# Kernel optimization log

Hardware: AMD Instinct MI355X
Metric: run time of the kernel (lower is better)

The kernel has to match this reference:

```python
import jax, jax.numpy as jnp
import numpy as np
import math

D_MODEL = 1024
N_HEADS = 16
D_K = D_MODEL // N_HEADS
WIDTH_MULTIPLIER = 1.0  # readout=False on all projections, so unused in math


def setup_inputs() -> dict:
    key = jax.random.key(0)
    kx, kq, kk, kv, ko = jax.random.split(key, 5)
    std = 1.0 / math.sqrt(D_MODEL)  # init_scale=1.0 / sqrt(in_features)
    x = jax.random.normal(kx, (2, 2048, D_MODEL), dtype=jnp.float32)
    # weights stored as (out_features, in_features), matching torch
    Wq = jax.random.normal(kq, (D_MODEL, D_MODEL), dtype=jnp.float32) * std
    Wk = jax.random.normal(kk, (D_MODEL, D_MODEL), dtype=jnp.float32) * std
    Wv = jax.random.normal(kv, (D_MODEL, D_MODEL), dtype=jnp.float32) * std
    Wo = jax.random.normal(ko, (D_MODEL, D_MODEL), dtype=jnp.float32) * std
    return {"x": x, "Wq": Wq, "Wk": Wk, "Wv": Wv, "Wo": Wo}


def reference(x, Wq, Wk, Wv, Wo):
    B, S, D = x.shape
    H, Dk = N_HEADS, D_K
    # muPLinear: x @ W.T (bias=False, readout=False)
    q = jnp.einsum('bsd,ed->bse', x, Wq).reshape(B, S, H, Dk).transpose(0, 2, 1, 3)
    k = jnp.einsum('bsd,ed->bse', x, Wk).reshape(B, S, H, Dk).transpose(0, 2, 1, 3)
    v = jnp.einsum('bsd,ed->bse', x, Wv).reshape(B, S, H, Dk).transpose(0, 2, 1, 3)
    # full [B,H,S,S] scores, scaled by 1/sqrt(d_k), softmax over keys
    scores = jnp.einsum('bhqd,bhkd->bhqk', q, k) / math.sqrt(Dk)
    attn = jax.nn.softmax(scores, axis=-1)
    out = jnp.einsum('bhqk,bhkd->bhqd', attn, v)
    out = out.transpose(0, 2, 1, 3).reshape(B, S, D)
    return jnp.einsum('bsd,ed->bse', out, Wo)
```

## Files before the change

kernel.cpp:

```cpp
#include <hip/hip_runtime.h>
#include <hip/hip_bf16.h>
#include <math.h>

#define D_MODEL 1024
#define N_HEADS 16
#define D_K     64
#define BATCH   2
#define SEQ     2048
#define M_TOTAL (BATCH * SEQ)

typedef __attribute__((ext_vector_type(8))) short short8;
typedef __attribute__((ext_vector_type(4))) float f32x4;
typedef __attribute__((ext_vector_type(16))) float f32x16;

__device__ __forceinline__ ushort f2bf(float f) {
    __hip_bfloat16 h = __float2bfloat16(f);
    union { __hip_bfloat16 h; ushort u; } c; c.h = h; return c.u;
}

__device__ __forceinline__ uint cvtpk(float a, float b) {
    uint r;
    asm("v_cvt_pk_bf16_f32 %0, %1, %2" : "=v"(r) : "v"(a), "v"(b));
    return r;
}

__device__ __forceinline__ void gload_lds16(const void* g, void* l) {
    __builtin_amdgcn_global_load_lds(
        (const __attribute__((address_space(1))) void*)g,
        (__attribute__((address_space(3))) void*)l, 16, 0, 0);
}

__device__ __forceinline__ void plswap(uint& a, uint& b) {
    asm volatile("v_permlane32_swap_b32 %0, %1" : "+v"(a), "+v"(b));
}

__global__ __launch_bounds__(256) void cast_all(const float* __restrict__ x,
                                                const float* __restrict__ Wq,
                                                const float* __restrict__ Wk,
                                                const float* __restrict__ Wv,
                                                const float* __restrict__ Wo,
                                                ushort* __restrict__ xb,
                                                ushort* __restrict__ wqkv,
                                                ushort* __restrict__ wob)
{
    const int bi = blockIdx.x;
    const float* src; ushort* dst; int blk;
    const int NW = D_MODEL * D_MODEL;
    if (bi < 4096)      { src = x;  dst = xb;            blk = bi; }
    else if (bi < 5120) { src = Wq; dst = wqkv;          blk = bi - 4096; }
    else if (bi < 6144) { src = Wk; dst = wqkv + NW;     blk = bi - 5120; }
    else if (bi < 7168) { src = Wv; dst = wqkv + 2 * NW; blk = bi - 6144; }
    else                { src = Wo; dst = wob;           blk = bi - 7168; }
    const int i = blk * 1024 + threadIdx.x * 4;
    float4 v = *(const float4*)&src[i];
    ushort4 o;
    o.x = f2bf(v.x); o.y = f2bf(v.y); o.z = f2bf(v.z); o.w = f2bf(v.w);
    *(ushort4*)&dst[i] = o;
}

template <int EPI>
__global__ __launch_bounds__(256) void gemm_bf16(const ushort* __restrict__ A,
                                                 const ushort* __restrict__ B,
                                                 void* __restrict__ C0,
                                                 void* __restrict__ C1,
                                                 void* __restrict__ C2,
                                                 int M, int N, int K)
{
    __shared__ ushort As[2][4 * 128 * 8];
    __shared__ ushort Bs[2][4 * 128 * 8];

    const int tid = threadIdx.x;
    const int lane = tid & 63;
    const int w = tid >> 6;
    const int li = lane & 15;
    const int kg = lane >> 4;

    const int nwg = gridDim.x * gridDim.y;
    const int flat = blockIdx.y * gridDim.x + blockIdx.x;
    const int cpx = nwg >> 3;
    const int swz = (flat & 7) * cpx + (flat >> 3);
    const int m0 = (swz / gridDim.x) * 128;
    const int n0 = (swz % gridDim.x) * 128;

    const int wr = (w >> 1) * 64;
    const int wc = (w & 1) * 64;

    f32x4 acc[4][4] = {};

    const int s1 = tid, s2 = tid + 256;
    const ushort* ga1 = &A[(size_t)(m0 + (s1 & 127)) * K + (s1 >> 7) * 8];
    const ushort* ga2 = &A[(size_t)(m0 + (s2 & 127)) * K + (s2 >> 7) * 8];
    const ushort* gb1 = &B[(size_t)(n0 + (s1 & 127)) * K + (s1 >> 7) * 8];
    const ushort* gb2 = &B[(size_t)(n0 + (s2 & 127)) * K + (s2 >> 7) * 8];

    const int NT = K / 32;
    gload_lds16(ga1, &As[0][s1 * 8]);
    gload_lds16(ga2, &As[0][s2 * 8]);
    gload_lds16(gb1, &Bs[0][s1 * 8]);
    gload_lds16(gb2, &Bs[0][s2 * 8]);

    for (int t = 0; t < NT; ++t) {
        const int cur = t & 1;
        asm volatile("s_waitcnt vmcnt(0)" ::: "memory");
        __syncthreads();
        if (t + 1 < NT) {
            const int kb = (t + 1) * 32;
            const int nxt = cur ^ 1;
            gload_lds16(ga1 + kb, &As[nxt][s1 * 8]);
            gload_lds16(ga2 + kb, &As[nxt][s2 * 8]);
            gload_lds16(gb1 + kb, &Bs[nxt][s1 * 8]);
            gload_lds16(gb2 + kb, &Bs[nxt][s2 * 8]);
        }
        short8 af[4], bf_[4];
#pragma unroll
        for (int m = 0; m < 4; ++m)
            af[m] = *(const short8*)&As[cur][(kg * 128 + wr + m * 16 + li) * 8];
#pragma unroll
        for (int n = 0; n < 4; ++n)
            bf_[n] = *(const short8*)&Bs[cur][(kg * 128 + wc + n * 16 + li) * 8];
#pragma unroll
        for (int m = 0; m < 4; ++m)
#pragma unroll
            for (int n = 0; n < 4; ++n)
                acc[m][n] = __builtin_amdgcn_mfma_f32_16x16x32_bf16(
                    af[m], bf_[n], acc[m][n], 0, 0, 0);
    }

    if (EPI == 1) {
        ushort* q = (ushort*)C0; ushort* k = (ushort*)C1; ushort* v = (ushort*)C2;
        const float QSCALE = 0.125f * 1.44269504088896f;
#pragma unroll
        for (int m = 0; m < 4; ++m) {
            const int Rb = m0 + wr + m * 16 + kg * 4;
#pragma unroll
            for (int n = 0; n < 4; ++n) {
                const int Ncol = n0 + wc + n * 16 + li;
                const int proj = Ncol >> 10;
                const int rem = Ncol & 1023;
                const int h = rem >> 6, dk = rem & 63;
#pragma unroll
                for (int r = 0; r < 4; ++r) {
                    const int R = Rb + r;
                    const int b = R >> 11, s = R & 2047;
                    const int bh = b * N_HEADS + h;
                    if (proj == 0)
                        q[((size_t)bh * SEQ + s) * D_K + dk] = f2bf(acc[m][n][r] * QSCALE);
                    else if (proj == 1)
                        k[((size_t)bh * SEQ + s) * D_K + dk] = f2bf(acc[m][n][r]);
                    else
                        v[((size_t)bh * D_K + dk) * SEQ + s] = f2bf(acc[m][n][r]);
                }
            }
        }
    } else {
        float* C = (float*)C0;
#pragma unroll
        for (int m = 0; m < 4; ++m) {
            const int Rb = m0 + wr + m * 16 + kg * 4;
#pragma unroll
            for (int n = 0; n < 4; ++n) {
                const int Ncol = n0 + wc + n * 16 + li;
#pragma unroll
                for (int r = 0; r < 4; ++r)
                    C[(size_t)(Rb + r) * N + Ncol] = acc[m][n][r];
            }
        }
    }
}

__global__ __launch_bounds__(512, 4) void attn_mfma(const ushort* __restrict__ Q,
                                                    const ushort* __restrict__ K,
                                                    const ushort* __restrict__ Vt,
                                                    ushort* __restrict__ AO)
{
    __shared__ ushort pool[2][2][2][64 * 64];

    const int tid = threadIdx.x, lane = tid & 63, w = tid >> 6;
    const int wq = w & 3, kvh = w >> 2;
    const int r31 = lane & 31, hi = lane >> 5;
    const int b = blockIdx.z, h = blockIdx.y, q0 = blockIdx.x * 128;
    const int bh = b * N_HEADS + h;
    const size_t base = (size_t)bh * SEQ * D_K;
    const size_t vbase = (size_t)bh * D_K * SEQ;

    uint pa = (uint)lane, pbv = 1000u + (uint)lane;
    plswap(pa, pbv);
    const bool swap_lo = (__builtin_amdgcn_readfirstlane(pa) > 500u);

    const size_t qrow = base + (size_t)(q0 + wq * 32 + r31) * D_K;
    short8 qb[4];
#pragma unroll
    for (int ks = 0; ks < 4; ++ks)
        qb[ks] = *(const short8*)&Q[qrow + ks * 16 + hi * 8];

    float m_ = -INFINITY, l_ = 0.f;
    f32x16 o0 = {}, o1 = {};

    const int srow_l = lane >> 3;
    const int sblk = lane & 7;
    const ushort* Kt0 = &K[base];
    const ushort* Vt0 = &Vt[vbase];
    const int tile0 = kvh * 16;

    const int xr = r31 & 7;
    int off[2][4];
#pragma unroll
    for (int hf = 0; hf < 2; ++hf)
#pragma unroll
        for (int ks = 0; ks < 4; ++ks)
            off[hf][ks] = hf * 2048 + r31 * 64 + (((2 * ks + hi) ^ xr) * 8);

    const ushort* Kst = &pool[kvh][0][0][0];
    const ushort* Vst = &pool[kvh][1][0][0];

#define STAGE(kt_, buf_)                                                       \
    {                                                                          \
        _Pragma("unroll")                                                      \
        for (int p = 0; p < 2; ++p) {                                          \
            const int row = wq * 16 + p * 8 + srow_l;                          \
            const int db = sblk ^ (row & 7);                                   \
            gload_lds16(Kt0 + ((size_t)((tile0 + (kt_)) * 64 + row)) * D_K + db * 8, \
                        &pool[kvh][0][buf_][(wq * 16 + p * 8) * 64]);          \
            gload_lds16(Vt0 + (size_t)row * SEQ + (tile0 + (kt_)) * 64 + db * 8,     \
                        &pool[kvh][1][buf_][(wq * 16 + p * 8) * 64]);          \
        }                                                                      \
    }

    STAGE(0, 0);

    const int NT = SEQ / 64 / 2;
    for (int kt = 0; kt < NT; ++kt) {
        const int cur = kt & 1;
        asm volatile("s_waitcnt vmcnt(0)" ::: "memory");
        __syncthreads();
        if (kt + 1 < NT) STAGE(kt + 1, cur ^ 1);
        const int cb = cur * 4096;

        f32x16 s0 = {}, s1 = {};
        __builtin_amdgcn_s_setprio(1);
#pragma unroll
        for (int ks = 0; ks < 4; ++ks) {
            short8 kb = *(const short8*)(Kst + cb + off[0][ks]);
            s0 = __builtin_amdgcn_mfma_f32_32x32x16_bf16(kb, qb[ks], s0, 0, 0, 0);
        }
#pragma unroll
        for (int ks = 0; ks < 4; ++ks) {
            short8 kb = *(const short8*)(Kst + cb + off[1][ks]);
            s1 = __builtin_amdgcn_mfma_f32_32x32x16_bf16(kb, qb[ks], s1, 0, 0, 0);
        }
        __builtin_amdgcn_s_setprio(0);

        float mx = fmaxf(s0[0], s0[1]);
#pragma unroll
        for (int e = 2; e < 16; ++e) mx = fmaxf(mx, s0[e]);
#pragma unroll
        for (int e = 0; e < 16; ++e) mx = fmaxf(mx, s1[e]);
        mx = fmaxf(mx, __shfl_xor(mx, 32, 64));

        if (__any(mx > m_ + 8.0f)) {
            const float mn = fmaxf(m_, mx);
            const float sc = exp2f(m_ - mn);
            l_ *= sc;
#pragma unroll
            for (int e = 0; e < 16; ++e) { o0[e] *= sc; o1[e] *= sc; }
            m_ = mn;
        }

        f32x16 p0, p1;
        float ts = 0.f;
#pragma unroll
        for (int e = 0; e < 16; ++e) { p0[e] = exp2f(s0[e] - m_); ts += p0[e]; }
#pragma unroll
        for (int e = 0; e < 16; ++e) { p1[e] = exp2f(s1[e] - m_); ts += p1[e]; }
        ts += __shfl_xor(ts, 32, 64);
        l_ += ts;

        uint u[8][2];
#pragma unroll
        for (int rq = 0; rq < 4; ++rq) {
            u[rq][0]     = cvtpk(p0[4 * rq + 0], p0[4 * rq + 1]);
            u[rq][1]     = cvtpk(p0[4 * rq + 2], p0[4 * rq + 3]);
            u[4 + rq][0] = cvtpk(p1[4 * rq + 0], p1[4 * rq + 1]);
            u[4 + rq][1] = cvtpk(p1[4 * rq + 2], p1[4 * rq + 3]);
        }

        short8 pb[4];
#pragma unroll
        for (int ks = 0; ks < 4; ++ks) {
            uint x0 = u[2 * ks][0], x1 = u[2 * ks][1];
            uint y0 = u[2 * ks + 1][0], y1 = u[2 * ks + 1][1];
            if (swap_lo) { plswap(y0, x0); plswap(y1, x1); }
            else         { plswap(x0, y0); plswap(x1, y1); }
            union { uint u4[4]; short8 s; } pu;
            pu.u4[0] = x0; pu.u4[1] = x1; pu.u4[2] = y0; pu.u4[3] = y1;
            pb[ks] = pu.s;
        }

        __builtin_amdgcn_s_setprio(1);
#pragma unroll
        for (int ks = 0; ks < 4; ++ks) {
            short8 vb = *(const short8*)(Vst + cb + off[0][ks]);
            o0 = __builtin_amdgcn_mfma_f32_32x32x16_bf16(vb, pb[ks], o0, 0, 0, 0);
        }
#pragma unroll
        for (int ks = 0; ks < 4; ++ks) {
            short8 vb = *(const short8*)(Vst + cb + off[1][ks]);
            o1 = __builtin_amdgcn_mfma_f32_32x32x16_bf16(vb, pb[ks], o1, 0, 0, 0);
        }
        __builtin_amdgcn_s_setprio(0);
    }
#undef STAGE

    __syncthreads();
    float* cs = (float*)&pool[0][0][0][0];
    float* ml = cs + 4 * 64 * 32;
    const int cidx = (wq * 64 + lane) * 32;
    if (kvh == 1) {
#pragma unroll
        for (int rq = 0; rq < 4; ++rq) {
            f32x4 a, c;
#pragma unroll
            for (int e = 0; e < 4; ++e) { a[e] = o0[4 * rq + e]; c[e] = o1[4 * rq + e]; }
            *(f32x4*)&cs[cidx + 4 * rq] = a;
            *(f32x4*)&cs[cidx + 16 + 4 * rq] = c;
        }
        ml[(wq * 64 + lane) * 2]     = m_;
        ml[(wq * 64 + lane) * 2 + 1] = l_;
    }
    __syncthreads();
    if (kvh == 0) {
        const float m2 = ml[(wq * 64 + lane) * 2];
        const float l2 = ml[(wq * 64 + lane) * 2 + 1];
        const float mM = fmaxf(m_, m2);
        const float sc1 = exp2f(m_ - mM), sc2 = exp2f(m2 - mM);
        const float linv = 1.f / (l_ * sc1 + l2 * sc2);
        ushort* Ao = &AO[((size_t)b * SEQ + q0 + wq * 32 + r31) * D_MODEL + h * 64];
#pragma unroll
        for (int rq = 0; rq < 4; ++rq) {
            f32x4 a = *(const f32x4*)&cs[cidx + 4 * rq];
            f32x4 c = *(const f32x4*)&cs[cidx + 16 + 4 * rq];
            uint2 v0, v1;
            v0.x = cvtpk((o0[4 * rq + 0] * sc1 + a[0] * sc2) * linv,
                         (o0[4 * rq + 1] * sc1 + a[1] * sc2) * linv);
            v0.y = cvtpk((o0[4 * rq + 2] * sc1 + a[2] * sc2) * linv,
                         (o0[4 * rq + 3] * sc1 + a[3] * sc2) * linv);
            v1.x = cvtpk((o1[4 * rq + 0] * sc1 + c[0] * sc2) * linv,
                         (o1[4 * rq + 1] * sc1 + c[1] * sc2) * linv);
            v1.y = cvtpk((o1[4 * rq + 2] * sc1 + c[2] * sc2) * linv,
                         (o1[4 * rq + 3] * sc1 + c[3] * sc2) * linv);
            *(uint2*)&Ao[8 * rq + 4 * hi]      = v0;
            *(uint2*)&Ao[32 + 8 * rq + 4 * hi] = v1;
        }
    }
}

extern "C" void kernel_launch(void* const* d_in, const int* in_sizes, int n_in,
                              void* d_out, int out_size, void* d_ws, size_t ws_size,
                              hipStream_t stream)
{
    const float* x  = (const float*)d_in[0];
    const float* Wq = (const float*)d_in[1];
    const float* Wk = (const float*)d_in[2];
    const float* Wv = (const float*)d_in[3];
    const float* Wo = (const float*)d_in[4];
    float* out = (float*)d_out;

    ushort* xb   = (ushort*)d_ws;
    ushort* Wqkv = xb + (size_t)M_TOTAL * D_MODEL;
    ushort* Wob  = Wqkv + (size_t)3 * D_MODEL * D_MODEL;
    ushort* q    = Wob + (size_t)D_MODEL * D_MODEL;
    ushort* k    = q + (size_t)M_TOTAL * D_MODEL;
    ushort* vt   = k + (size_t)M_TOTAL * D_MODEL;
    ushort* ao   = vt + (size_t)M_TOTAL * D_MODEL;

    hipLaunchKernelGGL(cast_all, dim3(8192), dim3(256), 0, stream,
                       x, Wq, Wk, Wv, Wo, xb, Wqkv, Wob);

    hipLaunchKernelGGL((gemm_bf16<1>), dim3(3 * D_MODEL / 128, M_TOTAL / 128), dim3(256),
                       0, stream, xb, Wqkv, q, k, vt, M_TOTAL, 3 * D_MODEL, D_MODEL);

    hipLaunchKernelGGL(attn_mfma, dim3(SEQ / 128, N_HEADS, BATCH), dim3(512),
                       0, stream, q, k, vt, ao);

    hipLaunchKernelGGL((gemm_bf16<0>), dim3(D_MODEL / 128, M_TOTAL / 128), dim3(256),
                       0, stream, ao, Wob, out, (void*)0, (void*)0,
                       M_TOTAL, D_MODEL, D_MODEL);
}
```

Before: 166.8 us.

## Stage V-transpose epilogue through LDS and shrink output GEMM tile to 64 rows

In the QKV projection GEMM, the V-projection tiles now write their accumulators into a swizzled LDS buffer and then emit the transposed V layout with coalesced 16-byte stores. Previously each element was a scattered 2-byte store strided by SEQ. The output projection GEMM becomes a separate kernel with 64x128 tiles. That doubles its workgroup count from 256 to 512 to improve CU occupancy on the small N=1024 problem. The cost is an extra LDS round trip and two barriers in the V epilogue, plus lower per-block reuse in the output GEMM.

```diff
diff --git a/kernel.cpp b/kernel.cpp
--- a/kernel.cpp
+++ b/kernel.cpp
@@ -58,22 +58,20 @@
     *(ushort4*)&dst[i] = o;
 }
 
-template <int EPI>
-__global__ __launch_bounds__(256) void gemm_bf16(const ushort* __restrict__ A,
-                                                 const ushort* __restrict__ B,
-                                                 void* __restrict__ C0,
-                                                 void* __restrict__ C1,
-                                                 void* __restrict__ C2,
-                                                 int M, int N, int K)
+__global__ __launch_bounds__(256) void gemm_qkv(const ushort* __restrict__ A,
+                                                const ushort* __restrict__ B,
+                                                ushort* __restrict__ q,
+                                                ushort* __restrict__ k,
+                                                ushort* __restrict__ v,
+                                                int M, int N, int K)
 {
-    __shared__ ushort As[2][4 * 128 * 8];
-    __shared__ ushort Bs[2][4 * 128 * 8];
+    __shared__ ushort SH[16384];
 
     const int tid = threadIdx.x;
     const int lane = tid & 63;
     const int w = tid >> 6;
     const int li = lane & 15;
-    const int kg = lane >> 4;
+    const int kgl = lane >> 4;
 
     const int nwg = gridDim.x * gridDim.y;
     const int flat = blockIdx.y * gridDim.x + blockIdx.x;
@@ -94,10 +92,10 @@
     const ushort* gb2 = &B[(size_t)(n0 + (s2 & 127)) * K + (s2 >> 7) * 8];
 
     const int NT = K / 32;
-    gload_lds16(ga1, &As[0][s1 * 8]);
-    gload_lds16(ga2, &As[0][s2 * 8]);
-    gload_lds16(gb1, &Bs[0][s1 * 8]);
-    gload_lds16(gb2, &Bs[0][s2 * 8]);
+    gload_lds16(ga1, &SH[0 + s1 * 8]);
+    gload_lds16(ga2, &SH[0 + s2 * 8]);
+    gload_lds16(gb1, &SH[8192 + s1 * 8]);
+    gload_lds16(gb2, &SH[8192 + s2 * 8]);
 
     for (int t = 0; t < NT; ++t) {
         const int cur = t & 1;
@@ -106,18 +104,18 @@
         if (t + 1 < NT) {
             const int kb = (t + 1) * 32;
             const int nxt = cur ^ 1;
-            gload_lds16(ga1 + kb, &As[nxt][s1 * 8]);
-            gload_lds16(ga2 + kb, &As[nxt][s2 * 8]);
-            gload_lds16(gb1 + kb, &Bs[nxt][s1 * 8]);
-            gload_lds16(gb2 + kb, &Bs[nxt][s2 * 8]);
+            gload_lds16(ga1 + kb, &SH[nxt * 4096 + s1 * 8]);
+            gload_lds16(ga2 + kb, &SH[nxt * 4096 + s2 * 8]);
+            gload_lds16(gb1 + kb, &SH[8192 + nxt * 4096 + s1 * 8]);
+            gload_lds16(gb2 + kb, &SH[8192 + nxt * 4096 + s2 * 8]);
         }
         short8 af[4], bf_[4];
 #pragma unroll
         for (int m = 0; m < 4; ++m)
-            af[m] = *(const short8*)&As[cur][(kg * 128 + wr + m * 16 + li) * 8];
+            af[m] = *(const short8*)&SH[cur * 4096 + (kgl * 128 + wr + m * 16 + li) * 8];
 #pragma unroll
         for (int n = 0; n < 4; ++n)
-            bf_[n] = *(const short8*)&Bs[cur][(kg * 128 + wc + n * 16 + li) * 8];
+            bf_[n] = *(const short8*)&SH[8192 + cur * 4096 + (kgl * 128 + wc + n * 16 + li) * 8];
 #pragma unroll
         for (int m = 0; m < 4; ++m)
 #pragma unroll
@@ -126,12 +124,11 @@
                     af[m], bf_[n], acc[m][n], 0, 0, 0);
     }
 
-    if (EPI == 1) {
-        ushort* q = (ushort*)C0; ushort* k = (ushort*)C1; ushort* v = (ushort*)C2;
+    if (n0 < 2048) {
         const float QSCALE = 0.125f * 1.44269504088896f;
 #pragma unroll
         for (int m = 0; m < 4; ++m) {
-            const int Rb = m0 + wr + m * 16 + kg * 4;
+            const int Rb = m0 + wr + m * 16 + kgl * 4;
 #pragma unroll
             for (int n = 0; n < 4; ++n) {
                 const int Ncol = n0 + wc + n * 16 + li;
@@ -145,25 +142,112 @@
                     const int bh = b * N_HEADS + h;
                     if (proj == 0)
                         q[((size_t)bh * SEQ + s) * D_K + dk] = f2bf(acc[m][n][r] * QSCALE);
-                    else if (proj == 1)
+                    else
                         k[((size_t)bh * SEQ + s) * D_K + dk] = f2bf(acc[m][n][r]);
-                    else
-                        v[((size_t)bh * D_K + dk) * SEQ + s] = f2bf(acc[m][n][r]);
                 }
             }
         }
     } else {
-        float* C = (float*)C0;
+        __syncthreads();
 #pragma unroll
         for (int m = 0; m < 4; ++m) {
-            const int Rb = m0 + wr + m * 16 + kg * 4;
+            const int row0 = wr + m * 16 + kgl * 4;
 #pragma unroll
             for (int n = 0; n < 4; ++n) {
-                const int Ncol = n0 + wc + n * 16 + li;
-#pragma unroll
-                for (int r = 0; r < 4; ++r)
-                    C[(size_t)(Rb + r) * N + Ncol] = acc[m][n][r];
+                const int col = wc + n * 16 + li;
+                uint2 pv;
+                pv.x = cvtpk(acc[m][n][0], acc[m][n][1]);
+                pv.y = cvtpk(acc[m][n][2], acc[m][n][3]);
+                const int byte = (col * 256 + row0 * 2) ^ ((col & 7) << 5);
+                *(uint2*)((char*)SH + byte) = pv;
             }
+        }
+        __syncthreads();
+        const int b = m0 >> 11, s0 = m0 & 2047;
+        const int lsl = tid & 15;
+        const int crow = tid >> 4;
+#pragma unroll
+        for (int it = 0; it < 8; ++it) {
+            const int c = it * 16 + crow;
+            const int rem = (n0 & 1023) + c;
+            const int h = rem >> 6, dk = rem & 63;
+            const int byte = (c * 256 + lsl * 16) ^ ((c & 7) << 5);
+            uint4 val = *(uint4*)((char*)SH + byte);
+            ushort* vp = v + ((size_t)(b * N_HEADS + h) * D_K + dk) * SEQ + s0 + lsl * 8;
+            *(uint4*)vp = val;
+        }
+    }
+}
+
+__global__ __launch_bounds__(256) void gemm_out(const ushort* __restrict__ A,
+                                                const ushort* __restrict__ B,
+                                                float* __restrict__ C,
+                                                int M, int N, int K)
+{
+    __shared__ ushort As[2][4 * 64 * 8];
+    __shared__ ushort Bs[2][4 * 128 * 8];
+
+    const int tid = threadIdx.x;
+    const int lane = tid & 63;
+    const int wv = tid >> 6;
+    const int li = lane & 15;
+    const int kgl = lane >> 4;
+
+    const int nwg = gridDim.x * gridDim.y;
+    const int flat = blockIdx.y * gridDim.x + blockIdx.x;
+    const int cpx = nwg >> 3;
+    const int swz = (flat & 7) * cpx + (flat >> 3);
+    const int m0 = (swz / gridDim.x) * 64;
+    const int n0 = (swz % gridDim.x) * 128;
+
+    f32x4 acc[4][2] = {};
+
+    const int sA = tid;
+    const int s1 = tid, s2 = tid + 256;
+    const ushort* gA  = &A[(size_t)(m0 + (sA & 63)) * K + (sA >> 6) * 8];
+    const ushort* gb1 = &B[(size_t)(n0 + (s1 & 127)) * K + (s1 >> 7) * 8];
+    const ushort* gb2 = &B[(size_t)(n0 + (s2 & 127)) * K + (s2 >> 7) * 8];
+
+    const int NT = K / 32;
+    gload_lds16(gA,  &As[0][sA * 8]);
+    gload_lds16(gb1, &Bs[0][s1 * 8]);
+    gload_lds16(gb2, &Bs[0][s2 * 8]);
+
+    for (int t = 0; t < NT; ++t) {
+        const int cur = t & 1;
+        asm volatile("s_waitcnt vmcnt(0)" ::: "memory");
+        __syncthreads();
+        if (t + 1 < NT) {
+            const int kb = (t + 1) * 32;
+            const int nxt = cur ^ 1;
+            gload_lds16(gA + kb,  &As[nxt][sA * 8]);
+            gload_lds16(gb1 + kb, &Bs[nxt][s1 * 8]);
+            gload_lds16(gb2 + kb, &Bs[nxt][s2 * 8]);
+        }
+        short8 af[4], bf_[2];
+#pragma unroll
+        for (int m = 0; m < 4; ++m)
+            af[m] = *(const short8*)&As[cur][(kgl * 64 + m * 16 + li) * 8];
+#pragma unroll
+        for (int n = 0; n < 2; ++n)
+            bf_[n] = *(const short8*)&Bs[cur][(kgl * 128 + wv * 32 + n * 16 + li) * 8];
+#pragma unroll
+        for (int m = 0; m < 4; ++m)
+#pragma unroll
+            for (int n = 0; n < 2; ++n)
+                acc[m][n] = __builtin_amdgcn_mfma_f32_16x16x32_bf16(
+                    af[m], bf_[n], acc[m][n], 0, 0, 0);
+    }
+
+#pragma unroll
+    for (int m = 0; m < 4; ++m) {
+        const int Rb = m0 + m * 16 + kgl * 4;
+#pragma unroll
+        for (int n = 0; n < 2; ++n) {
+            const int Ncol = n0 + wv * 32 + n * 16 + li;
+#pragma unroll
+            for (int r = 0; r < 4; ++r)
+                C[(size_t)(Rb + r) * N + Ncol] = acc[m][n][r];
         }
     }
 }
@@ -376,13 +460,12 @@
     hipLaunchKernelGGL(cast_all, dim3(8192), dim3(256), 0, stream,
                        x, Wq, Wk, Wv, Wo, xb, Wqkv, Wob);
 
-    hipLaunchKernelGGL((gemm_bf16<1>), dim3(3 * D_MODEL / 128, M_TOTAL / 128), dim3(256),
+    hipLaunchKernelGGL(gemm_qkv, dim3(3 * D_MODEL / 128, M_TOTAL / 128), dim3(256),
                        0, stream, xb, Wqkv, q, k, vt, M_TOTAL, 3 * D_MODEL, D_MODEL);
 
     hipLaunchKernelGGL(attn_mfma, dim3(SEQ / 128, N_HEADS, BATCH), dim3(512),
                        0, stream, q, k, vt, ao);
 
-    hipLaunchKernelGGL((gemm_bf16<0>), dim3(D_MODEL / 128, M_TOTAL / 128), dim3(256),
-                       0, stream, ao, Wob, out, (void*)0, (void*)0,
-                       M_TOTAL, D_MODEL, D_MODEL);
-}
+    hipLaunchKernelGGL(gemm_out, dim3(D_MODEL / 128, M_TOTAL / 64), dim3(256),
+                       0, stream, ao, Wob, out, M_TOTAL, D_MODEL, D_MODEL);
+}
```

Result: faster. 157.2 us (-5.7%).
